# Kernel optimization log

Hardware: AMD Instinct MI355X
Metric: run time of the kernel (lower is better)

The kernel has to match this reference:

```python
import jax, jax.numpy as jnp
import numpy as np

B, S, T, D = 4, 2, 1024, 512
H = 8
HD = D // H
EPS = 1e-6
LN_EPS = 1e-5


def setup_inputs() -> dict:
    key = jax.random.key(0)
    ks = jax.random.split(key, 12)
    def lin(k, fan_in, shape):
        bound = 1.0 / np.sqrt(fan_in)
        return jax.random.uniform(k, shape, jnp.float32, -bound, bound)
    return {
        "hidden_states": jax.random.normal(ks[0], (B, S, T, D), jnp.float32),
        "Wq": lin(ks[1], D, (D, D)), "bq": lin(ks[2], D, (D,)),
        "Wk": lin(ks[3], D, (D, D)), "bk": lin(ks[4], D, (D,)),
        "Wv": lin(ks[5], D, (D, D)), "bv": lin(ks[6], D, (D,)),
        "Wo": lin(ks[7], D, (D, D)), "bo": lin(ks[8], D, (D,)),
        "ln_g": jnp.ones((S, D), jnp.float32),
        "ln_b": jnp.zeros((S, D), jnp.float32),
        "gate_alpha": jnp.full((S,), 0.01, jnp.float32),
    }


def _heads(x):
    # [B,T,D] -> [B,H,T,HD]
    return x.reshape(B, T, H, HD).transpose(0, 2, 1, 3)


def _layernorm(x, g, b):
    mu = jnp.mean(x, axis=-1, keepdims=True)
    var = jnp.var(x, axis=-1, keepdims=True)
    return (x - mu) * jax.lax.rsqrt(var + LN_EPS) * g + b


def reference(hidden_states, Wq, bq, Wk, bk, Wv, bv, Wo, bo, ln_g, ln_b, gate_alpha):
    h1, h2 = hidden_states[:, 0], hidden_states[:, 1]  # [B,T,D]
    proj = lambda x, W, b: jnp.einsum('btd,ed->bte', x, W) + b
    Q1, K1, V1 = _heads(proj(h1, Wq, bq)), _heads(proj(h1, Wk, bk)), _heads(proj(h1, Wv, bv))
    Q2, K2, V2 = _heads(proj(h2, Wq, bq)), _heads(proj(h2, Wk, bk)), _heads(proj(h2, Wv, bv))
    scale = 1.0 / np.sqrt(HD)
    L12 = jnp.einsum('bhqd,bhkd->bhqk', Q1, K2) * scale
    L21 = jnp.einsum('bhqd,bhkd->bhqk', Q2, K1) * scale
    S12 = jax.nn.softmax(L12, axis=-1)
    S21 = jax.nn.softmax(L21, axis=-1)
    M = S12 + S21 + EPS
    A12 = S12 / M
    A21 = S21 / M
    H1 = jnp.einsum('bhqk,bhkd->bhqd', A12, V2).transpose(0, 2, 1, 3).reshape(B, T, D)
    H2 = jnp.einsum('bhqk,bhkd->bhqd', A21, V1).transpose(0, 2, 1, 3).reshape(B, T, D)
    H1 = _layernorm(jnp.einsum('btd,ed->bte', H1, Wo) + bo, ln_g[0], ln_b[0])
    H2 = _layernorm(jnp.einsum('btd,ed->bte', H2, Wo) + bo, ln_g[1], ln_b[1])
    attn = jnp.stack([H1, H2], axis=1)  # [B,2,T,D]
    return hidden_states + attn * gate_alpha[None, :, None, None]
```

## Files before the change

### kernel.cpp

```cpp
#include <hip/hip_runtime.h>

#define DEVI __device__ __forceinline__

typedef __bf16 v8bf __attribute__((ext_vector_type(8)));
typedef float  v4f  __attribute__((ext_vector_type(4)));
typedef short  v4s  __attribute__((ext_vector_type(4)));

DEVI unsigned short f2bf(float f) {
  unsigned u = __builtin_bit_cast(unsigned, f);
  u += 0x7fffu + ((u >> 16) & 1u);
  return (unsigned short)(u >> 16);
}
DEVI v4f MFMA32(v8bf a, v8bf b, v4f c) {
  return __builtin_amdgcn_mfma_f32_16x16x32_bf16(a, b, c, 0, 0, 0);
}
DEVI v8bf ldfrag(const unsigned short* p) {
  return __builtin_bit_cast(v8bf, *(const uint4*)p);
}
DEVI v4s ld4s(const unsigned short* p) {
  return __builtin_bit_cast(v4s, *(const uint2*)p);
}
DEVI unsigned pkbf(float lo, float hi) {
  unsigned a = __builtin_bit_cast(unsigned, hi) + 0x8000u;
  unsigned b = __builtin_bit_cast(unsigned, lo) + 0x8000u;
  return __builtin_amdgcn_perm(a, b, 0x07060302u);
}
DEVI float lo2f(unsigned u) { return __builtin_bit_cast(float, u << 16); }
DEVI float hi2f(unsigned u) { return __builtin_bit_cast(float, u & 0xffff0000u); }

DEVI void drain_vmem() { asm volatile("s_waitcnt vmcnt(0)" ::: "memory"); }

#if __has_builtin(__builtin_amdgcn_exp2f)
DEVI float fexp2(float x) { return __builtin_amdgcn_exp2f(x); }
#else
DEVI float fexp2(float x) { return exp2f(x); }
#endif

#if __has_builtin(__builtin_amdgcn_mfma_f32_16x16x16bf16_1k)
#define HAVE_MFMA16 1
DEVI v4f MFMA16(v4s a, v4s b, v4f c) {
  return __builtin_amdgcn_mfma_f32_16x16x16bf16_1k(a, b, c, 0, 0, 0);
}
#else
#define HAVE_MFMA16 0
#endif

#if __has_builtin(__builtin_amdgcn_global_load_lds)
DEVI void g2l(const unsigned short* g, unsigned short* l) {
  __builtin_amdgcn_global_load_lds(
      (const __attribute__((address_space(1))) unsigned int*)g,
      (__attribute__((address_space(3))) unsigned int*)l, 16, 0, 0);
}
#else
DEVI void g2l(const unsigned short* g, unsigned short* l) {
  *(uint4*)((char*)l + (threadIdx.x & 63) * 16) = *(const uint4*)g;
}
#endif

__global__ __launch_bounds__(256) void convert_kernel(
    const float* __restrict__ X, const float* __restrict__ Wq,
    const float* __restrict__ Wk, const float* __restrict__ Wv,
    const float* __restrict__ Wo, unsigned short* __restrict__ dst)
{
  int t = blockIdx.x * 256 + threadIdx.x;
  int idx = t * 4;
  const float* src;
  if (idx < 4194304) {
    src = X + idx;
  } else {
    int u = idx - 4194304;
    int w = u >> 18;
    const float* W = (w == 0) ? Wq : (w == 1) ? Wk : (w == 2) ? Wv : Wo;
    src = W + (u & 262143);
  }
  float4 f = *(const float4*)src;
  uint2 o;
  o.x = pkbf(f.x, f.y);
  o.y = pkbf(f.z, f.w);
  *(uint2*)&dst[idx] = o;
}

template<int OUTM, int BM>
__global__ __launch_bounds__(256) void gemm_bt(
    const unsigned short* __restrict__ A,
    const unsigned short* __restrict__ W0, const unsigned short* __restrict__ W1,
    const unsigned short* __restrict__ W2,
    const float* __restrict__ b0, const float* __restrict__ b1, const float* __restrict__ b2,
    void* __restrict__ C0, void* __restrict__ C1, void* __restrict__ C2)
{
  const int K = 512, N = 512;
  const int MI = BM / 32;
  const int PER = (BM / 8 + 16) / 4;
  __shared__ unsigned short sAB[2][(BM + 128) * 64];
  const int z = blockIdx.z;
  const unsigned short* W = (z == 0) ? W0 : (z == 1) ? W1 : W2;
  const float* bias = (z == 0) ? b0 : (z == 1) ? b1 : b2;
  void* C = (z == 0) ? C0 : (z == 1) ? C1 : C2;

  const int tid = threadIdx.x;
  const int lane = tid & 63, wave = tid >> 6;
  const int l15 = lane & 15, quad = lane >> 4, swl = l15 & 7;
  const int lrow = lane >> 3;
  const int lc8 = ((lane & 7) ^ (lrow & 7)) * 8;
  const int wm = (wave >> 1) * (BM / 2), wn = (wave & 1) * 64;
  const int mbase = blockIdx.y * BM, nbase = blockIdx.x * 128;

  const unsigned short* gsrc[PER];
  int loff[PER];
#pragma unroll
  for (int t = 0; t < PER; t++) {
    int c = wave * PER + t;
    loff[t] = c * 512;
    if (c < BM / 8) gsrc[t] = A + (size_t)(mbase + c * 8 + lrow) * K + lc8;
    else            gsrc[t] = W + (size_t)(nbase + (c - BM / 8) * 8 + lrow) * K + lc8;
  }

  v4f acc[MI][4] = {};

#pragma unroll
  for (int t = 0; t < PER; t++) g2l(gsrc[t], &sAB[0][loff[t]]);

  for (int kt = 0; kt < K / 64; kt++) {
    drain_vmem();
    __syncthreads();
    if (kt < K / 64 - 1) {
#pragma unroll
      for (int t = 0; t < PER; t++)
        g2l(gsrc[t] + (kt + 1) * 64, &sAB[(kt + 1) & 1][loff[t]]);
    }
    const int bu = kt & 1;
#pragma unroll
    for (int s = 0; s < 2; s++) {
      v8bf af[MI], bf[4];
#pragma unroll
      for (int i = 0; i < MI; i++)
        af[i] = ldfrag(&sAB[bu][(wm + i * 16 + l15) * 64 + ((s * 4 + quad) ^ swl) * 8]);
#pragma unroll
      for (int j = 0; j < 4; j++)
        bf[j] = ldfrag(&sAB[bu][(BM + wn + j * 16 + l15) * 64 + ((s * 4 + quad) ^ swl) * 8]);
#pragma unroll
      for (int i = 0; i < MI; i++)
#pragma unroll
        for (int j = 0; j < 4; j++)
          acc[i][j] = MFMA32(af[i], bf[j], acc[i][j]);
    }
  }

#pragma unroll
  for (int i = 0; i < MI; i++)
#pragma unroll
    for (int j = 0; j < 4; j++) {
      int row0 = mbase + wm + i * 16 + quad * 4;
      int col = nbase + wn + j * 16 + l15;
      float v[4];
#pragma unroll
      for (int r = 0; r < 4; r++) v[r] = acc[i][j][r] + bias[col];
      if (OUTM == 1) {
#pragma unroll
        for (int r = 0; r < 4; r++) ((float*)C)[(size_t)(row0 + r) * N + col] = v[r];
      } else if (z == 2) {
        int bs = row0 >> 10, t0 = row0 & 1023;
        int hh = col >> 6, hd = col & 63;
        uint2 o;
        o.x = pkbf(v[0], v[1]);
        o.y = pkbf(v[2], v[3]);
        *(uint2*)&((unsigned short*)C)[(size_t)((bs * 8 + hh) * 64 + hd) * 1024 + t0] = o;
      } else {
#pragma unroll
        for (int r = 0; r < 4; r++)
          ((unsigned short*)C)[(size_t)(row0 + r) * N + col] = f2bf(v[r]);
      }
    }
}

__global__ __launch_bounds__(256, 2) void attn_kernel(
    const unsigned short* __restrict__ Qg, const unsigned short* __restrict__ Kg,
    const unsigned short* __restrict__ VTg, unsigned short* __restrict__ Hc)
{
  __shared__ unsigned short sK[2][2][64][64];
  __shared__ unsigned short sV[2][2][64][64];

  const int pair = blockIdx.x & 31;
  const int b = pair >> 3, h = pair & 7;
  const int qt = blockIdx.x >> 5;
  const int tid = threadIdx.x;
  const int lane = tid & 63, wave = tid >> 6;
  const int l15 = lane & 15, quad = lane >> 4, swl = l15 & 7;
  const int lrow = lane >> 3;
  const int lc8 = ((lane & 7) ^ (lrow & 7)) * 8;
  const int qbase = qt * 64 + wave * 16;
  const float S2 = 0.125f * 1.44269504f;

  const unsigned short* kgp[2];
  const unsigned short* vgp[2];
#pragma unroll
  for (int st = 0; st < 2; st++) {
    kgp[st] = Kg + (size_t)((b * 2 + st) * 1024) * 512 + h * 64;
    vgp[st] = VTg + (size_t)(((b * 2 + st) * 8 + h) * 64) * 1024;
  }

  v8bf qf[2][2];
#pragma unroll
  for (int d = 0; d < 2; d++)
#pragma unroll
    for (int s = 0; s < 2; s++) {
      int qrow = (b * 2 + d) * 1024 + qbase + l15;
      qf[d][s] = ldfrag(&Qg[(size_t)qrow * 512 + h * 64 + s * 32 + quad * 8]);
    }

  float lacc[2] = {0.f, 0.f};
  {
    const unsigned short* gA[4];
    unsigned short* lA[2][4];
#pragma unroll
    for (int t = 0; t < 4; t++) {
      int c = wave * 4 + t;
      gA[t] = kgp[c >> 3] + (size_t)((c & 7) * 8 + lrow) * 512 + lc8;
      lA[0][t] = &sK[0][c >> 3][(c & 7) * 8][0];
      lA[1][t] = &sK[1][c >> 3][(c & 7) * 8][0];
    }
#pragma unroll
    for (int t = 0; t < 4; t++) g2l(gA[t], lA[0][t]);

    for (int kt = 0; kt < 16; kt++) {
      __syncthreads();
      if (kt < 15) {
#pragma unroll
        for (int t = 0; t < 4; t++)
          g2l(gA[t] + (size_t)(kt + 1) * 32768, lA[(kt + 1) & 1][t]);
      }
      const int bu = kt & 1;
      v4f acc[2][4] = {};
#pragma unroll
      for (int s = 0; s < 2; s++)
#pragma unroll
        for (int d = 0; d < 2; d++)
#pragma unroll
          for (int j = 0; j < 4; j++) {
            v8bf kf = ldfrag(&sK[bu][1 - d][j * 16 + l15][((s * 4 + quad) ^ swl) * 8]);
            acc[d][j] = MFMA32(kf, qf[d][s], acc[d][j]);
          }
#pragma unroll
      for (int d = 0; d < 2; d++)
#pragma unroll
        for (int j = 0; j < 4; j++)
#pragma unroll
          for (int r = 0; r < 4; r++)
            lacc[d] += fexp2(acc[d][j][r] * S2);
    }
  }
  float ll[2];
#pragma unroll
  for (int d = 0; d < 2; d++) {
    float v = lacc[d];
    v += __shfl_xor(v, 16);
    v += __shfl_xor(v, 32);
    ll[d] = __log2f(v);
  }
  const float dll = ll[0] - ll[1];

  v4f oacc[2][4] = {};
  {
    const unsigned short* gB[8];
    unsigned short* lB[2][8];
    size_t stp[8];
#pragma unroll
    for (int t = 0; t < 8; t++) {
      int c = wave * 8 + t;
      if (c < 16) {
        gB[t] = kgp[c >> 3] + (size_t)((c & 7) * 8 + lrow) * 512 + lc8;
        stp[t] = 32768;
        lB[0][t] = &sK[0][c >> 3][(c & 7) * 8][0];
        lB[1][t] = &sK[1][c >> 3][(c & 7) * 8][0];
      } else {
        int cv = c - 16;
        gB[t] = vgp[cv >> 3] + (size_t)((cv & 7) * 8 + lrow) * 1024 + lc8;
        stp[t] = 64;
        lB[0][t] = &sV[0][cv >> 3][(cv & 7) * 8][0];
        lB[1][t] = &sV[1][cv >> 3][(cv & 7) * 8][0];
      }
    }
    __syncthreads();
#pragma unroll
    for (int t = 0; t < 8; t++) g2l(gB[t], lB[0][t]);

    for (int kt = 0; kt < 16; kt++) {
      __syncthreads();
      if (kt < 15) {
#pragma unroll
        for (int t = 0; t < 8; t++)
          g2l(gB[t] + (size_t)(kt + 1) * stp[t], lB[(kt + 1) & 1][t]);
      }
      const int bu = kt & 1;

      v4f acc[2][4] = {};
#pragma unroll
      for (int s = 0; s < 2; s++)
#pragma unroll
        for (int d = 0; d < 2; d++)
#pragma unroll
          for (int j = 0; j < 4; j++) {
            v8bf kf = ldfrag(&sK[bu][1 - d][j * 16 + l15][((s * 4 + quad) ^ swl) * 8]);
            acc[d][j] = MFMA32(kf, qf[d][s], acc[d][j]);
          }

#pragma unroll
      for (int j = 0; j < 4; j++) {
        float r0[4], r1[4];
#pragma unroll
        for (int r = 0; r < 4; r++) {
          float t = fmaf(acc[1][j][r] - acc[0][j][r], S2, dll);
          float ri = __builtin_amdgcn_rcpf(1.f + fexp2(t));
          r0[r] = ri;
          r1[r] = 1.f - ri;
        }
#if HAVE_MFMA16
        uint2 w0, w1;
        w0.x = pkbf(r0[0], r0[1]); w0.y = pkbf(r0[2], r0[3]);
        w1.x = pkbf(r1[0], r1[1]); w1.y = pkbf(r1[2], r1[3]);
        v4s af0 = __builtin_bit_cast(v4s, w0);
        v4s af1 = __builtin_bit_cast(v4s, w1);
        int vcol = ((j * 2 + (quad >> 1)) ^ swl) * 8 + (quad & 1) * 4;
#pragma unroll
        for (int nt = 0; nt < 4; nt++) {
          v4s vf0 = ld4s(&sV[bu][1][nt * 16 + l15][vcol]);
          v4s vf1 = ld4s(&sV[bu][0][nt * 16 + l15][vcol]);
          oacc[0][nt] = MFMA16(af0, vf0, oacc[0][nt]);
          oacc[1][nt] = MFMA16(af1, vf1, oacc[1][nt]);
        }
#else
#pragma unroll
        for (int d = 0; d < 2; d++) {
          float (&cb)[4] = (d == 0) ? r0 : r1;
          v8bf a;
#pragma unroll
          for (int jj = 0; jj < 8; jj++) {
            int src = l15 + 16 * ((jj >> 2) + (quad & 1) * 2);
            float v = __shfl(cb[jj & 3], src);
            a[jj] = __builtin_bit_cast(__bf16, f2bf(v));
          }
#pragma unroll
          for (int nt = 0; nt < 4; nt++) {
            v8bf vf = ldfrag(&sV[bu][1 - d][nt * 16 + l15]
                               [(((j & 2) * 2 + quad) ^ swl) * 8]);
            oacc[d][nt] = MFMA32(a, vf, oacc[d][nt]);
          }
        }
#endif
      }
    }
  }

#pragma unroll
  for (int d = 0; d < 2; d++)
#pragma unroll
    for (int nt = 0; nt < 4; nt++)
#pragma unroll
      for (int r = 0; r < 4; r++) {
        int row = (b * 2 + d) * 1024 + qbase + quad * 4 + r;
        int col = h * 64 + nt * 16 + l15;
        Hc[(size_t)row * 512 + col] = f2bf(oacc[d][nt][r]);
      }
}

__global__ __launch_bounds__(256) void ln_kernel(
    const unsigned short* __restrict__ Pb, const float* __restrict__ hidden,
    const float* __restrict__ ln_g, const float* __restrict__ ln_b,
    const float* __restrict__ gate, float* __restrict__ out)
{
  const int row = blockIdx.x * 4 + (threadIdx.x >> 6);
  const int s = (row >> 10) & 1;
  const int lane = threadIdx.x & 63;
  const int d0 = lane * 8;

  uint4 up = *(const uint4*)&Pb[(size_t)row * 512 + d0];
  float x[8] = { lo2f(up.x), hi2f(up.x), lo2f(up.y), hi2f(up.y),
                 lo2f(up.z), hi2f(up.z), lo2f(up.w), hi2f(up.w) };
  float s1 = 0.f, s2 = 0.f;
#pragma unroll
  for (int i = 0; i < 8; i++) { s1 += x[i]; s2 += x[i] * x[i]; }
#pragma unroll
  for (int m = 1; m < 64; m <<= 1) { s1 += __shfl_xor(s1, m); s2 += __shfl_xor(s2, m); }
  float mu = s1 * (1.f / 512.f);
  float var = s2 * (1.f / 512.f) - mu * mu;
  float rs = rsqrtf(var + 1e-5f);
  float al = gate[s];

  float4 h0 = *(const float4*)&hidden[(size_t)row * 512 + d0];
  float4 h1 = *(const float4*)&hidden[(size_t)row * 512 + d0 + 4];
  float4 g0 = *(const float4*)&ln_g[s * 512 + d0];
  float4 g1 = *(const float4*)&ln_g[s * 512 + d0 + 4];
  float4 bb0 = *(const float4*)&ln_b[s * 512 + d0];
  float4 bb1 = *(const float4*)&ln_b[s * 512 + d0 + 4];
  float4 o0, o1;
  o0.x = h0.x + ((x[0] - mu) * rs * g0.x + bb0.x) * al;
  o0.y = h0.y + ((x[1] - mu) * rs * g0.y + bb0.y) * al;
  o0.z = h0.z + ((x[2] - mu) * rs * g0.z + bb0.z) * al;
  o0.w = h0.w + ((x[3] - mu) * rs * g0.w + bb0.w) * al;
  o1.x = h1.x + ((x[4] - mu) * rs * g1.x + bb1.x) * al;
  o1.y = h1.y + ((x[5] - mu) * rs * g1.y + bb1.y) * al;
  o1.z = h1.z + ((x[6] - mu) * rs * g1.z + bb1.z) * al;
  o1.w = h1.w + ((x[7] - mu) * rs * g1.w + bb1.w) * al;
  *(float4*)&out[(size_t)row * 512 + d0] = o0;
  *(float4*)&out[(size_t)row * 512 + d0 + 4] = o1;
}

extern "C" void kernel_launch(void* const* d_in, const int* in_sizes, int n_in,
                              void* d_out, int out_size, void* d_ws, size_t ws_size,
                              hipStream_t stream)
{
  const float* hidden = (const float*)d_in[0];
  const float* Wq = (const float*)d_in[1];
  const float* bq = (const float*)d_in[2];
  const float* Wk = (const float*)d_in[3];
  const float* bk = (const float*)d_in[4];
  const float* Wv = (const float*)d_in[5];
  const float* bv = (const float*)d_in[6];
  const float* Wo = (const float*)d_in[7];
  const float* bo = (const float*)d_in[8];
  const float* ln_g = (const float*)d_in[9];
  const float* ln_b = (const float*)d_in[10];
  const float* gate = (const float*)d_in[11];

  unsigned short* U = (unsigned short*)d_ws;
  unsigned short* Xbf = U;
  unsigned short* Wqb = U + 4194304;
  unsigned short* Wkb = U + 4456448;
  unsigned short* Wvb = U + 4718592;
  unsigned short* Wob = U + 4980736;
  unsigned short* Qg  = U + 5242880;
  unsigned short* Kg  = U + 9437184;
  unsigned short* VT  = U + 13631488;
  unsigned short* Hc  = U + 17825792;
  unsigned short* Pb  = (unsigned short*)((char*)d_ws + 44302336);

  convert_kernel<<<dim3(5120), 256, 0, stream>>>(hidden, Wq, Wk, Wv, Wo, Xbf);
  gemm_bt<0, 128><<<dim3(4, 64, 3), 256, 0, stream>>>(Xbf, Wqb, Wkb, Wvb, bq, bk, bv, Qg, Kg, VT);
  attn_kernel<<<dim3(512), 256, 0, stream>>>(Qg, Kg, VT, Hc);
  gemm_bt<0, 64><<<dim3(4, 128, 1), 256, 0, stream>>>(Hc, Wob, Wob, Wob, bo, bo, bo, Pb, Pb, Pb);
  ln_kernel<<<dim3(2048), 256, 0, stream>>>(Pb, hidden, ln_g, ln_b, gate, (float*)d_out);
}
```

Measured before the change: 180.6 us.

## Load K/V fragments directly from global memory instead of LDS staging

Removes the shared-memory double-buffered K and V tiles and their per-iteration block barriers. Each wave now reads its MFMA fragments for K and V^T straight from global memory, relying on L1/L2 caching of data shared across the four waves. Launch bounds are raised to four blocks per CU, since LDS no longer limits occupancy. The trade-off is redundant global/cache traffic across waves and less latency hiding in exchange for no syncs or LDS usage.

```diff
diff --git a/kernel.cpp b/kernel.cpp
--- a/kernel.cpp
+++ b/kernel.cpp
@@ -173,30 +173,27 @@
     }
 }
 
-__global__ __launch_bounds__(256, 2) void attn_kernel(
+__global__ __launch_bounds__(256, 4) void attn_kernel(
     const unsigned short* __restrict__ Qg, const unsigned short* __restrict__ Kg,
     const unsigned short* __restrict__ VTg, unsigned short* __restrict__ Hc)
 {
-  __shared__ unsigned short sK[2][2][64][64];
-  __shared__ unsigned short sV[2][2][64][64];
-
   const int pair = blockIdx.x & 31;
   const int b = pair >> 3, h = pair & 7;
   const int qt = blockIdx.x >> 5;
   const int tid = threadIdx.x;
   const int lane = tid & 63, wave = tid >> 6;
-  const int l15 = lane & 15, quad = lane >> 4, swl = l15 & 7;
-  const int lrow = lane >> 3;
-  const int lc8 = ((lane & 7) ^ (lrow & 7)) * 8;
+  const int l15 = lane & 15, quad = lane >> 4;
   const int qbase = qt * 64 + wave * 16;
   const float S2 = 0.125f * 1.44269504f;
 
-  const unsigned short* kgp[2];
-  const unsigned short* vgp[2];
+  const unsigned short* kp[2];
+  const unsigned short* vp[2];
 #pragma unroll
   for (int st = 0; st < 2; st++) {
-    kgp[st] = Kg + (size_t)((b * 2 + st) * 1024) * 512 + h * 64;
-    vgp[st] = VTg + (size_t)(((b * 2 + st) * 8 + h) * 64) * 1024;
+    kp[st] = Kg + (size_t)((b * 2 + st) * 1024) * 512 + h * 64
+               + l15 * 512 + quad * 8;
+    vp[st] = VTg + (size_t)(((b * 2 + st) * 8 + h) * 64) * 1024
+               + l15 * 1024 + (quad >> 1) * 8 + (quad & 1) * 4;
   }
 
   v8bf qf[2][2];
@@ -209,44 +206,24 @@
     }
 
   float lacc[2] = {0.f, 0.f};
-  {
-    const unsigned short* gA[4];
-    unsigned short* lA[2][4];
-#pragma unroll
-    for (int t = 0; t < 4; t++) {
-      int c = wave * 4 + t;
-      gA[t] = kgp[c >> 3] + (size_t)((c & 7) * 8 + lrow) * 512 + lc8;
-      lA[0][t] = &sK[0][c >> 3][(c & 7) * 8][0];
-      lA[1][t] = &sK[1][c >> 3][(c & 7) * 8][0];
-    }
-#pragma unroll
-    for (int t = 0; t < 4; t++) g2l(gA[t], lA[0][t]);
-
-    for (int kt = 0; kt < 16; kt++) {
-      __syncthreads();
-      if (kt < 15) {
-#pragma unroll
-        for (int t = 0; t < 4; t++)
-          g2l(gA[t] + (size_t)(kt + 1) * 32768, lA[(kt + 1) & 1][t]);
-      }
-      const int bu = kt & 1;
-      v4f acc[2][4] = {};
-#pragma unroll
-      for (int s = 0; s < 2; s++)
-#pragma unroll
-        for (int d = 0; d < 2; d++)
-#pragma unroll
-          for (int j = 0; j < 4; j++) {
-            v8bf kf = ldfrag(&sK[bu][1 - d][j * 16 + l15][((s * 4 + quad) ^ swl) * 8]);
-            acc[d][j] = MFMA32(kf, qf[d][s], acc[d][j]);
-          }
+  for (int kt = 0; kt < 16; kt++) {
+    const unsigned short* k0 = kp[1] + kt * 32768;
+    const unsigned short* k1 = kp[0] + kt * 32768;
+#pragma unroll
+    for (int j = 0; j < 4; j++) {
+      v4f acc[2] = {};
+#pragma unroll
+      for (int s = 0; s < 2; s++) {
+        v8bf kf0 = ldfrag(k0 + j * 8192 + s * 32);
+        v8bf kf1 = ldfrag(k1 + j * 8192 + s * 32);
+        acc[0] = MFMA32(kf0, qf[0][s], acc[0]);
+        acc[1] = MFMA32(kf1, qf[1][s], acc[1]);
+      }
 #pragma unroll
       for (int d = 0; d < 2; d++)
 #pragma unroll
-        for (int j = 0; j < 4; j++)
-#pragma unroll
-          for (int r = 0; r < 4; r++)
-            lacc[d] += fexp2(acc[d][j][r] * S2);
+        for (int r = 0; r < 4; r++)
+          lacc[d] += fexp2(acc[d][r] * S2);
     }
   }
   float ll[2];
@@ -260,94 +237,64 @@
   const float dll = ll[0] - ll[1];
 
   v4f oacc[2][4] = {};
-  {
-    const unsigned short* gB[8];
-    unsigned short* lB[2][8];
-    size_t stp[8];
-#pragma unroll
-    for (int t = 0; t < 8; t++) {
-      int c = wave * 8 + t;
-      if (c < 16) {
-        gB[t] = kgp[c >> 3] + (size_t)((c & 7) * 8 + lrow) * 512 + lc8;
-        stp[t] = 32768;
-        lB[0][t] = &sK[0][c >> 3][(c & 7) * 8][0];
-        lB[1][t] = &sK[1][c >> 3][(c & 7) * 8][0];
-      } else {
-        int cv = c - 16;
-        gB[t] = vgp[cv >> 3] + (size_t)((cv & 7) * 8 + lrow) * 1024 + lc8;
-        stp[t] = 64;
-        lB[0][t] = &sV[0][cv >> 3][(cv & 7) * 8][0];
-        lB[1][t] = &sV[1][cv >> 3][(cv & 7) * 8][0];
-      }
-    }
-    __syncthreads();
-#pragma unroll
-    for (int t = 0; t < 8; t++) g2l(gB[t], lB[0][t]);
-
-    for (int kt = 0; kt < 16; kt++) {
-      __syncthreads();
-      if (kt < 15) {
-#pragma unroll
-        for (int t = 0; t < 8; t++)
-          g2l(gB[t] + (size_t)(kt + 1) * stp[t], lB[(kt + 1) & 1][t]);
-      }
-      const int bu = kt & 1;
-
-      v4f acc[2][4] = {};
-#pragma unroll
-      for (int s = 0; s < 2; s++)
-#pragma unroll
-        for (int d = 0; d < 2; d++)
-#pragma unroll
-          for (int j = 0; j < 4; j++) {
-            v8bf kf = ldfrag(&sK[bu][1 - d][j * 16 + l15][((s * 4 + quad) ^ swl) * 8]);
-            acc[d][j] = MFMA32(kf, qf[d][s], acc[d][j]);
-          }
-
-#pragma unroll
-      for (int j = 0; j < 4; j++) {
-        float r0[4], r1[4];
-#pragma unroll
-        for (int r = 0; r < 4; r++) {
-          float t = fmaf(acc[1][j][r] - acc[0][j][r], S2, dll);
-          float ri = __builtin_amdgcn_rcpf(1.f + fexp2(t));
-          r0[r] = ri;
-          r1[r] = 1.f - ri;
+  for (int kt = 0; kt < 16; kt++) {
+    const unsigned short* k0 = kp[1] + kt * 32768;
+    const unsigned short* k1 = kp[0] + kt * 32768;
+    const unsigned short* v0 = vp[1] + kt * 64;
+    const unsigned short* v1 = vp[0] + kt * 64;
+#pragma unroll
+    for (int j = 0; j < 4; j++) {
+      v4f acc[2] = {};
+#pragma unroll
+      for (int s = 0; s < 2; s++) {
+        v8bf kf0 = ldfrag(k0 + j * 8192 + s * 32);
+        v8bf kf1 = ldfrag(k1 + j * 8192 + s * 32);
+        acc[0] = MFMA32(kf0, qf[0][s], acc[0]);
+        acc[1] = MFMA32(kf1, qf[1][s], acc[1]);
+      }
+
+      float r0[4], r1[4];
+#pragma unroll
+      for (int r = 0; r < 4; r++) {
+        float t = fmaf(acc[1][r] - acc[0][r], S2, dll);
+        float ri = __builtin_amdgcn_rcpf(1.f + fexp2(t));
+        r0[r] = ri;
+        r1[r] = 1.f - ri;
+      }
+#if HAVE_MFMA16
+      uint2 w0, w1;
+      w0.x = pkbf(r0[0], r0[1]); w0.y = pkbf(r0[2], r0[3]);
+      w1.x = pkbf(r1[0], r1[1]); w1.y = pkbf(r1[2], r1[3]);
+      v4s af0 = __builtin_bit_cast(v4s, w0);
+      v4s af1 = __builtin_bit_cast(v4s, w1);
+#pragma unroll
+      for (int nt = 0; nt < 4; nt++) {
+        v4s vf0 = ld4s(v0 + nt * 16384 + j * 16);
+        v4s vf1 = ld4s(v1 + nt * 16384 + j * 16);
+        oacc[0][nt] = MFMA16(af0, vf0, oacc[0][nt]);
+        oacc[1][nt] = MFMA16(af1, vf1, oacc[1][nt]);
+      }
+#else
+#pragma unroll
+      for (int d = 0; d < 2; d++) {
+        float (&cb)[4] = (d == 0) ? r0 : r1;
+        v8bf a;
+#pragma unroll
+        for (int jj = 0; jj < 8; jj++) {
+          int src = l15 + 16 * ((jj >> 2) + (quad & 1) * 2);
+          float v = __shfl(cb[jj & 3], src);
+          a[jj] = __builtin_bit_cast(__bf16, f2bf(v));
         }
-#if HAVE_MFMA16
-        uint2 w0, w1;
-        w0.x = pkbf(r0[0], r0[1]); w0.y = pkbf(r0[2], r0[3]);
-        w1.x = pkbf(r1[0], r1[1]); w1.y = pkbf(r1[2], r1[3]);
-        v4s af0 = __builtin_bit_cast(v4s, w0);
-        v4s af1 = __builtin_bit_cast(v4s, w1);
-        int vcol = ((j * 2 + (quad >> 1)) ^ swl) * 8 + (quad & 1) * 4;
+        const unsigned short* vq = VTg
+            + (size_t)(((b * 2 + (1 - d)) * 8 + h) * 64) * 1024
+            + l15 * 1024 + kt * 64 + ((j & 2) * 2 + quad) * 8;
 #pragma unroll
         for (int nt = 0; nt < 4; nt++) {
-          v4s vf0 = ld4s(&sV[bu][1][nt * 16 + l15][vcol]);
-          v4s vf1 = ld4s(&sV[bu][0][nt * 16 + l15][vcol]);
-          oacc[0][nt] = MFMA16(af0, vf0, oacc[0][nt]);
-          oacc[1][nt] = MFMA16(af1, vf1, oacc[1][nt]);
+          v8bf vf = ldfrag(vq + nt * 16384);
+          oacc[d][nt] = MFMA32(a, vf, oacc[d][nt]);
         }
-#else
-#pragma unroll
-        for (int d = 0; d < 2; d++) {
-          float (&cb)[4] = (d == 0) ? r0 : r1;
-          v8bf a;
-#pragma unroll
-          for (int jj = 0; jj < 8; jj++) {
-            int src = l15 + 16 * ((jj >> 2) + (quad & 1) * 2);
-            float v = __shfl(cb[jj & 3], src);
-            a[jj] = __builtin_bit_cast(__bf16, f2bf(v));
-          }
-#pragma unroll
-          for (int nt = 0; nt < 4; nt++) {
-            v8bf vf = ldfrag(&sV[bu][1 - d][nt * 16 + l15]
-                               [(((j & 2) * 2 + quad) ^ swl) * 8]);
-            oacc[d][nt] = MFMA32(a, vf, oacc[d][nt]);
-          }
-        }
+      }
 #endif
-      }
     }
   }
 
```

New measurement: 364.2 us. 102% more time.

## Split attention into separate softmax-normalizer pass with key-halved parallelism

Applied to the files above, without the earlier changes.

The fused attention kernel is split into two launches. The first computes the per-row softmax denominators, splits the keys into two halves across twice as many blocks, raises the occupancy hint to 4, and writes partial sums to a small workspace. The second kernel reads and combines those sums and then runs the main pass. This aims to fill the GPU better during the normalizer phase, at the cost of an extra launch, reloading Q and a small global round-trip. It also adds explicit vmem drains before the barriers and drops a barrier that is no longer needed.

```diff
diff --git a/kernel.cpp b/kernel.cpp
--- a/kernel.cpp
+++ b/kernel.cpp
@@ -173,9 +173,102 @@
     }
 }
 
-__global__ __launch_bounds__(256, 2) void attn_kernel(
+__global__ __launch_bounds__(256, 4) void attn_a(
     const unsigned short* __restrict__ Qg, const unsigned short* __restrict__ Kg,
-    const unsigned short* __restrict__ VTg, unsigned short* __restrict__ Hc)
+    float* __restrict__ Lws)
+{
+  __shared__ unsigned short sK[2][2][64][64];
+
+  const int pair = blockIdx.x & 31;
+  const int b = pair >> 3, h = pair & 7;
+  const int qt = (blockIdx.x >> 5) & 15;
+  const int kh = blockIdx.x >> 9;
+  const int tid = threadIdx.x;
+  const int lane = tid & 63, wave = tid >> 6;
+  const int l15 = lane & 15, quad = lane >> 4, swl = l15 & 7;
+  const int lrow = lane >> 3;
+  const int lc8 = ((lane & 7) ^ (lrow & 7)) * 8;
+  const int qbase = qt * 64 + wave * 16;
+  const float S2 = 0.125f * 1.44269504f;
+
+  const unsigned short* kgp[2];
+#pragma unroll
+  for (int st = 0; st < 2; st++)
+    kgp[st] = Kg + (size_t)((b * 2 + st) * 1024) * 512 + h * 64;
+
+  v8bf qf[2][2];
+#pragma unroll
+  for (int d = 0; d < 2; d++)
+#pragma unroll
+    for (int s = 0; s < 2; s++) {
+      int qrow = (b * 2 + d) * 1024 + qbase + l15;
+      qf[d][s] = ldfrag(&Qg[(size_t)qrow * 512 + h * 64 + s * 32 + quad * 8]);
+    }
+
+  const unsigned short* gA[4];
+  unsigned short* lA[2][4];
+#pragma unroll
+  for (int t = 0; t < 4; t++) {
+    int c = wave * 4 + t;
+    gA[t] = kgp[c >> 3] + (size_t)((c & 7) * 8 + lrow) * 512 + lc8
+            + (size_t)kh * 262144;
+    lA[0][t] = &sK[0][c >> 3][(c & 7) * 8][0];
+    lA[1][t] = &sK[1][c >> 3][(c & 7) * 8][0];
+  }
+
+  float lacc[2] = {0.f, 0.f};
+#pragma unroll
+  for (int t = 0; t < 4; t++) g2l(gA[t], lA[0][t]);
+
+  for (int kt = 0; kt < 8; kt++) {
+    drain_vmem();
+    __syncthreads();
+    if (kt < 7) {
+#pragma unroll
+      for (int t = 0; t < 4; t++)
+        g2l(gA[t] + (size_t)(kt + 1) * 32768, lA[(kt + 1) & 1][t]);
+    }
+    const int bu = kt & 1;
+    v4f acc[2][4] = {};
+#pragma unroll
+    for (int s = 0; s < 2; s++)
+#pragma unroll
+      for (int d = 0; d < 2; d++)
+#pragma unroll
+        for (int j = 0; j < 4; j++) {
+          v8bf kf = ldfrag(&sK[bu][1 - d][j * 16 + l15][((s * 4 + quad) ^ swl) * 8]);
+          acc[d][j] = MFMA32(kf, qf[d][s], acc[d][j]);
+        }
+#pragma unroll
+    for (int d = 0; d < 2; d++)
+#pragma unroll
+      for (int j = 0; j < 4; j++)
+#pragma unroll
+        for (int r = 0; r < 4; r++)
+          lacc[d] += fexp2(acc[d][j][r] * S2);
+  }
+
+  float lv[2];
+#pragma unroll
+  for (int d = 0; d < 2; d++) {
+    float v = lacc[d];
+    v += __shfl_xor(v, 16);
+    v += __shfl_xor(v, 32);
+    lv[d] = v;
+  }
+  if (quad == 0) {
+#pragma unroll
+    for (int d = 0; d < 2; d++) {
+      int qrow = (b * 2 + d) * 1024 + qbase + l15;
+      Lws[(size_t)qrow * 2 + kh] = lv[d];
+    }
+  }
+}
+
+__global__ __launch_bounds__(256, 2) void attn_b(
+    const unsigned short* __restrict__ Qg, const unsigned short* __restrict__ Kg,
+    const unsigned short* __restrict__ VTg, const float* __restrict__ Lws,
+    unsigned short* __restrict__ Hc)
 {
   __shared__ unsigned short sK[2][2][64][64];
   __shared__ unsigned short sV[2][2][64][64];
@@ -208,54 +301,12 @@
       qf[d][s] = ldfrag(&Qg[(size_t)qrow * 512 + h * 64 + s * 32 + quad * 8]);
     }
 
-  float lacc[2] = {0.f, 0.f};
-  {
-    const unsigned short* gA[4];
-    unsigned short* lA[2][4];
-#pragma unroll
-    for (int t = 0; t < 4; t++) {
-      int c = wave * 4 + t;
-      gA[t] = kgp[c >> 3] + (size_t)((c & 7) * 8 + lrow) * 512 + lc8;
-      lA[0][t] = &sK[0][c >> 3][(c & 7) * 8][0];
-      lA[1][t] = &sK[1][c >> 3][(c & 7) * 8][0];
-    }
-#pragma unroll
-    for (int t = 0; t < 4; t++) g2l(gA[t], lA[0][t]);
-
-    for (int kt = 0; kt < 16; kt++) {
-      __syncthreads();
-      if (kt < 15) {
-#pragma unroll
-        for (int t = 0; t < 4; t++)
-          g2l(gA[t] + (size_t)(kt + 1) * 32768, lA[(kt + 1) & 1][t]);
-      }
-      const int bu = kt & 1;
-      v4f acc[2][4] = {};
-#pragma unroll
-      for (int s = 0; s < 2; s++)
-#pragma unroll
-        for (int d = 0; d < 2; d++)
-#pragma unroll
-          for (int j = 0; j < 4; j++) {
-            v8bf kf = ldfrag(&sK[bu][1 - d][j * 16 + l15][((s * 4 + quad) ^ swl) * 8]);
-            acc[d][j] = MFMA32(kf, qf[d][s], acc[d][j]);
-          }
-#pragma unroll
-      for (int d = 0; d < 2; d++)
-#pragma unroll
-        for (int j = 0; j < 4; j++)
-#pragma unroll
-          for (int r = 0; r < 4; r++)
-            lacc[d] += fexp2(acc[d][j][r] * S2);
-    }
-  }
   float ll[2];
 #pragma unroll
   for (int d = 0; d < 2; d++) {
-    float v = lacc[d];
-    v += __shfl_xor(v, 16);
-    v += __shfl_xor(v, 32);
-    ll[d] = __log2f(v);
+    int qrow = (b * 2 + d) * 1024 + qbase + l15;
+    float2 p = *(const float2*)&Lws[(size_t)qrow * 2];
+    ll[d] = __log2f(p.x + p.y);
   }
   const float dll = ll[0] - ll[1];
 
@@ -280,11 +331,11 @@
         lB[1][t] = &sV[1][cv >> 3][(cv & 7) * 8][0];
       }
     }
-    __syncthreads();
 #pragma unroll
     for (int t = 0; t < 8; t++) g2l(gB[t], lB[0][t]);
 
     for (int kt = 0; kt < 16; kt++) {
+      drain_vmem();
       __syncthreads();
       if (kt < 15) {
 #pragma unroll
@@ -433,10 +484,12 @@
   unsigned short* VT  = U + 13631488;
   unsigned short* Hc  = U + 17825792;
   unsigned short* Pb  = (unsigned short*)((char*)d_ws + 44302336);
+  float* Lws = (float*)d_ws;
 
   convert_kernel<<<dim3(5120), 256, 0, stream>>>(hidden, Wq, Wk, Wv, Wo, Xbf);
   gemm_bt<0, 128><<<dim3(4, 64, 3), 256, 0, stream>>>(Xbf, Wqb, Wkb, Wvb, bq, bk, bv, Qg, Kg, VT);
-  attn_kernel<<<dim3(512), 256, 0, stream>>>(Qg, Kg, VT, Hc);
+  attn_a<<<dim3(1024), 256, 0, stream>>>(Qg, Kg, Lws);
+  attn_b<<<dim3(512), 256, 0, stream>>>(Qg, Kg, VT, Lws, Hc);
   gemm_bt<0, 64><<<dim3(4, 128, 1), 256, 0, stream>>>(Hc, Wob, Wob, Wob, bo, bo, bo, Pb, Pb, Pb);
   ln_kernel<<<dim3(2048), 256, 0, stream>>>(Pb, hidden, ln_g, ln_b, gate, (float*)d_out);
 }
```

After: 176.5 us. 2.3% less time.
